# Kernel optimization log

Hardware: AMD Instinct MI355X
Metric: run time of the kernel (lower is better)

Reference implementation:

```python
import jax, jax.numpy as jnp
import numpy as np

SIGMA = 1.0  # init kwarg: Gaussian kernel width

B, P, F = 8192, 8192, 256


def setup_inputs() -> dict:
    key = jax.random.key(0)
    kx, kp = jax.random.split(key)
    x = jax.random.normal(kx, (B, F), dtype=jnp.float32)
    prototypes = jax.random.normal(kp, (P, F), dtype=jnp.float32)
    return {"x": x, "prototypes": prototypes}


def reference(x, prototypes):
    x_sq = jnp.sum(x * x, axis=-1, keepdims=True)            # [B,1]
    p_sq = jnp.sum(prototypes * prototypes, axis=-1)          # [P]
    cross = jnp.einsum('bf,pf->bp', x, prototypes)            # [B,P]
    d2 = jnp.maximum(x_sq + p_sq[None, :] - 2.0 * cross, 0.0)
    # NOTE: original takes .pow(0.5) -> euclidean NORM (despite variable name)
    dist = jnp.sqrt(d2)                                       # [B,P]
    denom = jnp.float32(2.0 * SIGMA ** 2)
    return jnp.exp(-dist / denom)
```

## Files before the change

### kernel.cpp

```cpp
#include <hip/hip_runtime.h>
#include <cstdint>
#include <cstddef>

#define B_ROWS 8192
#define P_ROWS 8192
#define FDIM   256

#define BM 128
#define BN 128
#define BK 64
#define NSTEP (FDIM / BK)

typedef __bf16  bf16x8  __attribute__((ext_vector_type(8)));
typedef float   floatx4 __attribute__((ext_vector_type(4)));

__device__ __forceinline__ unsigned short f2bf(float f) {
  unsigned int u = __float_as_uint(f);
  u += 0x7fffu + ((u >> 16) & 1u);
  return (unsigned short)(u >> 16);
}

__device__ __forceinline__ void async16(const void* g, void* l) {
  __builtin_amdgcn_global_load_lds(
      (const __attribute__((address_space(1))) void*)g,
      (__attribute__((address_space(3))) void*)l,
      16, 0, 0);
}

__global__ void __launch_bounds__(64) prep_kernel(
    const float* __restrict__ x, const float* __restrict__ p,
    unsigned short* __restrict__ xbf, unsigned short* __restrict__ pbf,
    float* __restrict__ x2, float* __restrict__ p2) {
  const int row  = blockIdx.x;
  const int lane = threadIdx.x;

  const float* src;
  unsigned short* dst;
  float* nrm;
  int r;
  if (row < B_ROWS) { src = x; dst = xbf; nrm = x2; r = row; }
  else              { src = p; dst = pbf; nrm = p2; r = row - B_ROWS; }

  const float4 v = *reinterpret_cast<const float4*>(src + (size_t)r * FDIM + lane * 4);
  float s = v.x * v.x + v.y * v.y + v.z * v.z + v.w * v.w;
  #pragma unroll
  for (int o = 32; o > 0; o >>= 1) s += __shfl_down(s, o);
  if (lane == 0) nrm[r] = s;

  ushort4 pk;
  pk.x = f2bf(v.x); pk.y = f2bf(v.y); pk.z = f2bf(v.z); pk.w = f2bf(v.w);
  *reinterpret_cast<ushort4*>(dst + (size_t)r * FDIM + lane * 4) = pk;
}

__global__ void __launch_bounds__(256) gauss_kernel(
    const unsigned short* __restrict__ xbf, const unsigned short* __restrict__ pbf,
    const float* __restrict__ x2, const float* __restrict__ p2,
    float* __restrict__ out) {
  __shared__ __align__(16) unsigned short lds_a[BM * BK];
  __shared__ __align__(16) unsigned short lds_b[BN * BK];

  const int t    = threadIdx.x;
  const int lane = t & 63;
  const int w    = t >> 6;
  const int wr   = w >> 1;
  const int wc   = w & 1;
  const int lm   = lane & 15;
  const int q    = lane >> 4;
  const int sx   = lane & 7;

  const int M0 = blockIdx.y * BM;
  const int N0 = blockIdx.x * BN;

  const unsigned short* aSrc[4];
  const unsigned short* bSrc[4];
  int ldsOff[4];
  #pragma unroll
  for (int I = 0; I < 4; ++I) {
    const int L = I * 256 + w * 64 + lane;
    const int r = L >> 3;
    const int c = L & 7;
    const int g = c ^ (r & 7);
    aSrc[I] = xbf + (size_t)(M0 + r) * FDIM + g * 8;
    bSrc[I] = pbf + (size_t)(N0 + r) * FDIM + g * 8;
    ldsOff[I] = (I * 256 + w * 64) * 8;
  }

  floatx4 acc[4][4] = {};

  for (int s = 0; s < NSTEP; ++s) {
    __syncthreads();
    #pragma unroll
    for (int I = 0; I < 4; ++I) async16(aSrc[I] + s * BK, &lds_a[ldsOff[I]]);
    #pragma unroll
    for (int I = 0; I < 4; ++I) async16(bSrc[I] + s * BK, &lds_b[ldsOff[I]]);
    __syncthreads();

    #pragma unroll
    for (int kk = 0; kk < 2; ++kk) {
      const int slot = ((kk * 4 + q) ^ sx) * 8;
      const int aoff = (wr * 64 + lm) * BK + slot;
      const int boff = (wc * 64 + lm) * BK + slot;
      bf16x8 af[4], bfr[4];
      #pragma unroll
      for (int i = 0; i < 4; ++i) af[i]  = *(const bf16x8*)&lds_a[aoff + i * 16 * BK];
      #pragma unroll
      for (int j = 0; j < 4; ++j) bfr[j] = *(const bf16x8*)&lds_b[boff + j * 16 * BK];
      #pragma unroll
      for (int i = 0; i < 4; ++i)
        #pragma unroll
        for (int j = 0; j < 4; ++j)
          acc[i][j] = __builtin_amdgcn_mfma_f32_16x16x32_bf16(af[i], bfr[j], acc[i][j], 0, 0, 0);
    }
  }

  float p2r[4];
  #pragma unroll
  for (int j = 0; j < 4; ++j) p2r[j] = p2[N0 + wc * 64 + j * 16 + lm];
  float x2r[16];
  #pragma unroll
  for (int i = 0; i < 4; ++i)
    #pragma unroll
    for (int v = 0; v < 4; ++v)
      x2r[i * 4 + v] = x2[M0 + wr * 64 + i * 16 + q * 4 + v];

  #pragma unroll
  for (int i = 0; i < 4; ++i) {
    const int mbase = M0 + wr * 64 + i * 16 + q * 4;
    #pragma unroll
    for (int v = 0; v < 4; ++v) {
      float* orow = out + (size_t)(mbase + v) * P_ROWS + N0 + wc * 64 + lm;
      #pragma unroll
      for (int j = 0; j < 4; ++j) {
        float d2 = x2r[i * 4 + v] + p2r[j] - 2.0f * acc[i][j][v];
        d2 = fmaxf(d2, 0.0f);
        const float dist = sqrtf(d2);
        orow[j * 16] = __expf(-0.5f * dist);
      }
    }
  }
}

extern "C" void kernel_launch(void* const* d_in, const int* in_sizes, int n_in,
                              void* d_out, int out_size, void* d_ws, size_t ws_size,
                              hipStream_t stream) {
  const float* x = (const float*)d_in[0];
  const float* p = (const float*)d_in[1];
  float* out = (float*)d_out;

  char* ws = (char*)d_ws;
  unsigned short* xbf = (unsigned short*)ws;
  unsigned short* pbf = (unsigned short*)(ws + (size_t)B_ROWS * FDIM * 2);
  float* x2 = (float*)(ws + (size_t)(B_ROWS + P_ROWS) * FDIM * 2);
  float* p2 = x2 + B_ROWS;

  prep_kernel<<<dim3(B_ROWS + P_ROWS), dim3(64), 0, stream>>>(x, p, xbf, pbf, x2, p2);

  dim3 grid(P_ROWS / BN, B_ROWS / BM);
  gauss_kernel<<<grid, dim3(256), 0, stream>>>(xbf, pbf, x2, p2, out);
}
```

Measured before the change: 303.8 us.

## Stage epilogue through LDS for float4 stores, swizzle tile order, batch prep rows

The epilogue now writes each wave's 16x64 output sub-tile into padded LDS, reusing the A/B tile buffers, then reads it back and stores full 16-byte float4 rows to global memory instead of scattered 4-byte stores. Output tiles are remapped so 8x8 groups of blocks run together, improving L2 reuse of the x and prototype tiles. The prep kernel now handles four rows per 256-thread block to cut the block count. The cost is an extra barrier and an LDS round trip per output sub-tile.

```diff
diff --git a/kernel.cpp b/kernel.cpp
--- a/kernel.cpp
+++ b/kernel.cpp
@@ -27,12 +27,13 @@
       16, 0, 0);
 }
 
-__global__ void __launch_bounds__(64) prep_kernel(
+__global__ void __launch_bounds__(256) prep_kernel(
     const float* __restrict__ x, const float* __restrict__ p,
     unsigned short* __restrict__ xbf, unsigned short* __restrict__ pbf,
     float* __restrict__ x2, float* __restrict__ p2) {
-  const int row  = blockIdx.x;
-  const int lane = threadIdx.x;
+  const int t    = threadIdx.x;
+  const int lane = t & 63;
+  const int row  = blockIdx.x * 4 + (t >> 6);
 
   const float* src;
   unsigned short* dst;
@@ -68,8 +69,10 @@
   const int q    = lane >> 4;
   const int sx   = lane & 7;
 
-  const int M0 = blockIdx.y * BM;
-  const int N0 = blockIdx.x * BN;
+  const int sid = blockIdx.x >> 6;
+  const int wit = blockIdx.x & 63;
+  const int M0 = ((sid >> 3) * 8 + (wit >> 3)) * BM;
+  const int N0 = ((sid &  7) * 8 + (wit &  7)) * BN;
 
   const unsigned short* aSrc[4];
   const unsigned short* bSrc[4];
@@ -113,6 +116,11 @@
     }
   }
 
+  __syncthreads();
+
+  float* wbase = (w < 2) ? ((float*)lds_a + w * 1088)
+                         : ((float*)lds_b + (w - 2) * 1088);
+
   float p2r[4];
   #pragma unroll
   for (int j = 0; j < 4; ++j) p2r[j] = p2[N0 + wc * 64 + j * 16 + lm];
@@ -125,17 +133,19 @@
 
   #pragma unroll
   for (int i = 0; i < 4; ++i) {
-    const int mbase = M0 + wr * 64 + i * 16 + q * 4;
     #pragma unroll
-    for (int v = 0; v < 4; ++v) {
-      float* orow = out + (size_t)(mbase + v) * P_ROWS + N0 + wc * 64 + lm;
+    for (int j = 0; j < 4; ++j)
       #pragma unroll
-      for (int j = 0; j < 4; ++j) {
-        float d2 = x2r[i * 4 + v] + p2r[j] - 2.0f * acc[i][j][v];
-        d2 = fmaxf(d2, 0.0f);
-        const float dist = sqrtf(d2);
-        orow[j * 16] = __expf(-0.5f * dist);
+      for (int v = 0; v < 4; ++v) {
+        float d2 = fmaxf(x2r[i * 4 + v] + p2r[j] - 2.0f * acc[i][j][v], 0.0f);
+        wbase[(q * 4 + v) * 68 + j * 16 + lm] = __expf(-0.5f * sqrtf(d2));
       }
+    const int mbase = M0 + wr * 64 + i * 16;
+    #pragma unroll
+    for (int tt = 0; tt < 4; ++tt) {
+      const int r2 = q + tt * 4;
+      const float4 vv = *(const float4*)&wbase[r2 * 68 + lm * 4];
+      *(float4*)(out + (size_t)(mbase + r2) * P_ROWS + N0 + wc * 64 + lm * 4) = vv;
     }
   }
 }
@@ -153,8 +163,7 @@
   float* x2 = (float*)(ws + (size_t)(B_ROWS + P_ROWS) * FDIM * 2);
   float* p2 = x2 + B_ROWS;
 
-  prep_kernel<<<dim3(B_ROWS + P_ROWS), dim3(64), 0, stream>>>(x, p, xbf, pbf, x2, p2);
+  prep_kernel<<<dim3((B_ROWS + P_ROWS) / 4), dim3(256), 0, stream>>>(x, p, xbf, pbf, x2, p2);
 
-  dim3 grid(P_ROWS / BN, B_ROWS / BM);
-  gauss_kernel<<<grid, dim3(256), 0, stream>>>(xbf, pbf, x2, p2, out);
+  gauss_kernel<<<dim3(64 * 64), dim3(256), 0, stream>>>(xbf, pbf, x2, p2, out);
 }
```

New measurement: 311.3 us. +2.5%, slower.
